# Kernel optimization log

Measured on AMD Instinct MI355X. Metric: run time of the kernel, lower is better.

## Reference

```python
import jax, jax.numpy as jnp
import numpy as np

STRIDES = {"feat1": 4, "feat2": 8, "feat3": 16}
ROI_SIZES = {"feat1": 28, "feat2": 14, "feat3": 7}
SAMPLING_RATIO = 2


def roi_align(feat, rois, out_size, spatial_scale, ratio):
    """torchvision roi_align with aligned=True, fixed sampling_ratio.
    feat: (B,C,H,W); rois: (N,5) [batch_idx,x1,y1,x2,y2]. Returns (N,C,P,P)."""
    B, C, H, W = feat.shape
    bidx = rois[:, 0].astype(jnp.int32)
    # aligned=True: half-pixel offset
    x1 = rois[:, 1] * spatial_scale - 0.5
    y1 = rois[:, 2] * spatial_scale - 0.5
    x2 = rois[:, 3] * spatial_scale - 0.5
    y2 = rois[:, 4] * spatial_scale - 0.5
    bin_h = (y2 - y1) / out_size
    bin_w = (x2 - x1) / out_size
    # per-bin sampling grid offsets: (P, r)
    grid = jnp.arange(out_size, dtype=feat.dtype)[:, None] + \
        (jnp.arange(ratio, dtype=feat.dtype)[None, :] + 0.5) / ratio
    ys = y1[:, None, None] + grid[None] * bin_h[:, None, None]  # (N,P,ry)
    xs = x1[:, None, None] + grid[None] * bin_w[:, None, None]  # (N,P,rx)
    yy = ys[:, :, :, None, None]  # (N,P,ry,1,1)
    xx = xs[:, None, None, :, :]  # (N,1,1,P,rx)
    valid = (yy > -1.0) & (yy < H) & (xx > -1.0) & (xx < W)
    yc = jnp.clip(yy, 0.0, H - 1.0)
    xc = jnp.clip(xx, 0.0, W - 1.0)
    y0 = jnp.floor(yc).astype(jnp.int32)
    x0 = jnp.floor(xc).astype(jnp.int32)
    y1i = jnp.minimum(y0 + 1, H - 1)
    x1i = jnp.minimum(x0 + 1, W - 1)
    ly = yc - y0
    lx = xc - x0
    hy = 1.0 - ly
    hx = 1.0 - lx
    b = bidx[:, None, None, None, None]  # (N,1,1,1,1)

    def gather(yi, xi):
        # advanced indexing -> (N,P,ry,P,rx,C)
        return feat[b, :, yi, xi]

    v = ((hy * hx)[..., None] * gather(y0, x0)
         + (hy * lx)[..., None] * gather(y0, x1i)
         + (ly * hx)[..., None] * gather(y1i, x0)
         + (ly * lx)[..., None] * gather(y1i, x1i))
    v = jnp.where(valid[..., None], v, 0.0)
    out = v.mean(axis=(2, 4))  # average over sampling grid -> (N,P,P,C)
    return jnp.transpose(out, (0, 3, 1, 2))  # (N,C,P,P)


def setup_inputs() -> dict:
    key = jax.random.key(0)
    ks = jax.random.split(key, 6)
    B, C, N, IMG = 2, 256, 128, 1024
    feat1 = jax.random.normal(ks[0], (B, C, 256, 256), jnp.float32)
    feat2 = jax.random.normal(ks[1], (B, C, 128, 128), jnp.float32)
    feat3 = jax.random.normal(ks[2], (B, C, 64, 64), jnp.float32)
    bidx = jax.random.randint(ks[3], (N,), 0, B).astype(jnp.float32)
    xy1 = jax.random.uniform(ks[4], (N, 2), jnp.float32, 0.0, IMG - 64.0)
    wh = jax.random.uniform(ks[5], (N, 2), jnp.float32, 16.0, 320.0)
    xy2 = jnp.minimum(xy1 + wh, IMG - 1.0)
    rois = jnp.concatenate(
        [bidx[:, None], xy1[:, :1], xy1[:, 1:], xy2[:, :1], xy2[:, 1:]], axis=1)
    return {"feat1": feat1, "feat2": feat2, "feat3": feat3, "rois": rois}


def reference(feat1, feat2, feat3, rois):
    feats = {"feat1": feat1, "feat2": feat2, "feat3": feat3}
    return tuple(
        roi_align(feats[k], rois, ROI_SIZES[k], 1.0 / STRIDES[k], SAMPLING_RATIO)
        for k in ("feat1", "feat2", "feat3"))
```

## Files before the change

kernel.cpp:

```cpp
#include <hip/hip_runtime.h>

#define C_CH 256

__global__ __launch_bounds__(256) void nchw_to_nhwc(
    const float* __restrict__ in, float* __restrict__ out, int HW)
{
    __shared__ float lds[64 * 64];
    int ct = blockIdx.y & 3;
    int b  = blockIdx.y >> 2;
    int hw0 = blockIdx.x << 6;
    int c0  = ct << 6;
    const float* ip = in  + (size_t)b * C_CH * HW;
    float*       op = out + (size_t)b * HW * C_CH;

    int t   = threadIdx.x;
    int q   = t & 15;
    int r0  = t >> 4;

#pragma unroll
    for (int k = 0; k < 4; ++k) {
        int c_local = r0 + (k << 4);
        const float4 v = *reinterpret_cast<const float4*>(
            ip + (size_t)(c0 + c_local) * HW + hw0 + (q << 2));
#pragma unroll
        for (int i = 0; i < 4; ++i) {
            int hw_local = (q << 2) + i;
            lds[(hw_local << 6) + ((c_local + hw_local) & 63)] = ((const float*)&v)[i];
        }
    }
    __syncthreads();
#pragma unroll
    for (int k = 0; k < 4; ++k) {
        int hw_local = r0 + (k << 4);
        float4 v;
#pragma unroll
        for (int j = 0; j < 4; ++j) {
            int c_local = (q << 2) + j;
            ((float*)&v)[j] = lds[(hw_local << 6) + ((c_local + hw_local) & 63)];
        }
        *reinterpret_cast<float4*>(
            op + (size_t)(hw0 + hw_local) * C_CH + c0 + (q << 2)) = v;
    }
}

template<int P, int POS>
__global__ __launch_bounds__(256) void roi_gather_nhwc(
    const float* __restrict__ nhwc, const float* __restrict__ rois,
    float* __restrict__ out, int H, int W, float scale)
{
    constexpr int PITCH = 260;
    __shared__ float lds[POS * PITCH];

    const int n   = blockIdx.x;
    const int ph0 = blockIdx.y * (POS / P);
    const int lane = threadIdx.x & 63;
    const int wid  = threadIdx.x >> 6;
    const int c4   = lane << 2;

    const float* r = rois + n * 5;
    const int b = (int)r[0];
    const float x1 = fmaf(r[1], scale, -0.5f);
    const float y1 = fmaf(r[2], scale, -0.5f);
    const float x2 = fmaf(r[3], scale, -0.5f);
    const float y2 = fmaf(r[4], scale, -0.5f);
    const float bin_h = (y2 - y1) * (1.0f / P);
    const float bin_w = (x2 - x1) * (1.0f / P);

    const float Hm1 = (float)(H - 1), Wm1 = (float)(W - 1);
    const float Hf = (float)H, Wf = (float)W;
    const float* fb = nhwc + (size_t)b * H * W * C_CH;

    for (int pos = wid; pos < POS; pos += 4) {
        int ph = ph0 + pos / P;
        int pw = pos % P;

        float w[16];
        int   offc[16];
#pragma unroll
        for (int iy = 0; iy < 2; ++iy) {
            float gy = (float)ph + (iy ? 0.75f : 0.25f);
            float yy = fmaf(gy, bin_h, y1);
            bool vy = (yy > -1.0f) && (yy < Hf);
            float yc = fminf(fmaxf(yy, 0.0f), Hm1);
            float y0f = floorf(yc);
            int   y0  = (int)y0f;
            float ly  = yc - y0f, hy = 1.0f - ly;
            int   y1i = min(y0 + 1, H - 1);
            int ro0 = y0 * W, ro1 = y1i * W;
#pragma unroll
            for (int ix = 0; ix < 2; ++ix) {
                float gx = (float)pw + (ix ? 0.75f : 0.25f);
                float xx = fmaf(gx, bin_w, x1);
                bool v = vy && (xx > -1.0f) && (xx < Wf);
                float xc = fminf(fmaxf(xx, 0.0f), Wm1);
                float x0f = floorf(xc);
                int   x0  = (int)x0f;
                float lx  = xc - x0f, hx = 1.0f - lx;
                int   x1i = min(x0 + 1, W - 1);
                float q = v ? 0.25f : 0.0f;
                int s = ((iy << 1) + ix) << 2;
                w[s + 0] = hy * hx * q;  offc[s + 0] = ((ro0 + x0 ) << 8) + c4;
                w[s + 1] = hy * lx * q;  offc[s + 1] = ((ro0 + x1i) << 8) + c4;
                w[s + 2] = ly * hx * q;  offc[s + 2] = ((ro1 + x0 ) << 8) + c4;
                w[s + 3] = ly * lx * q;  offc[s + 3] = ((ro1 + x1i) << 8) + c4;
            }
        }

        float4 acc = {0.f, 0.f, 0.f, 0.f};
#pragma unroll
        for (int m = 0; m < 16; ++m) {
            const float4 v = *reinterpret_cast<const float4*>(fb + (size_t)(unsigned)offc[m]);
            acc.x = fmaf(w[m], v.x, acc.x);
            acc.y = fmaf(w[m], v.y, acc.y);
            acc.z = fmaf(w[m], v.z, acc.z);
            acc.w = fmaf(w[m], v.w, acc.w);
        }
        *reinterpret_cast<float4*>(&lds[pos * PITCH + c4]) = acc;
    }
    __syncthreads();

    const size_t obase = (size_t)n * C_CH * P * P + (size_t)ph0 * P;
    for (int i = threadIdx.x; i < C_CH * POS; i += 256) {
        int c = i / POS;
        int pos = i - c * POS;
        out[obase + (size_t)c * (P * P) + pos] = lds[pos * PITCH + c];
    }
}

template<int P, int CPT>
__global__ __launch_bounds__(256) void roi_align_direct(
    const float* __restrict__ feat, const float* __restrict__ rois,
    float* __restrict__ out, int N, int H, int W, float scale)
{
    constexpr int CG = C_CH / CPT;
    int tid = blockIdx.x * blockDim.x + threadIdx.x;
    int total = N * CG * P * P;
    if (tid >= total) return;

    int pw = tid % P;
    int t  = tid / P;
    int ph = t % P;
    t /= P;
    int cg = t % CG;
    int n  = t / CG;

    const float* r = rois + n * 5;
    int b = (int)r[0];
    float x1 = fmaf(r[1], scale, -0.5f);
    float y1 = fmaf(r[2], scale, -0.5f);
    float x2 = fmaf(r[3], scale, -0.5f);
    float y2 = fmaf(r[4], scale, -0.5f);
    float bin_h = (y2 - y1) * (1.0f / P);
    float bin_w = (x2 - x1) * (1.0f / P);

    float acc[CPT];
#pragma unroll
    for (int j = 0; j < CPT; ++j) acc[j] = 0.0f;

    const int HW = H * W;
    const float* fp = feat + ((size_t)b * C_CH + (size_t)cg * CPT) * HW;
    const float Hm1 = (float)(H - 1), Wm1 = (float)(W - 1);
    const float Hf = (float)H, Wf = (float)W;

#pragma unroll
    for (int iy = 0; iy < 2; ++iy) {
        float gy = (float)ph + (iy ? 0.75f : 0.25f);
        float yy = fmaf(gy, bin_h, y1);
        bool vy = (yy > -1.0f) && (yy < Hf);
        float yc = fminf(fmaxf(yy, 0.0f), Hm1);
        float y0f = floorf(yc);
        int   y0  = (int)y0f;
        float ly  = yc - y0f, hy = 1.0f - ly;
        int   y1i = min(y0 + 1, H - 1);
        int ro0 = y0 * W, ro1 = y1i * W;
#pragma unroll
        for (int ix = 0; ix < 2; ++ix) {
            float gx = (float)pw + (ix ? 0.75f : 0.25f);
            float xx = fmaf(gx, bin_w, x1);
            bool v = vy && (xx > -1.0f) && (xx < Wf);
            float xc = fminf(fmaxf(xx, 0.0f), Wm1);
            float x0f = floorf(xc);
            int   x0  = (int)x0f;
            float lx  = xc - x0f, hx = 1.0f - lx;
            int   x1i = min(x0 + 1, W - 1);
            float q = v ? 0.25f : 0.0f;
            float w00 = hy * hx * q, w01 = hy * lx * q;
            float w10 = ly * hx * q, w11 = ly * lx * q;
            int o00 = ro0 + x0, o01 = ro0 + x1i;
            int o10 = ro1 + x0, o11 = ro1 + x1i;
#pragma unroll
            for (int j = 0; j < CPT; ++j) {
                const float* pj = fp + j * HW;
                acc[j] = fmaf(w00, pj[o00], acc[j]);
                acc[j] = fmaf(w01, pj[o01], acc[j]);
                acc[j] = fmaf(w10, pj[o10], acc[j]);
                acc[j] = fmaf(w11, pj[o11], acc[j]);
            }
        }
    }

    float* op = out + (((size_t)n * C_CH + (size_t)cg * CPT) * P + ph) * P + pw;
#pragma unroll
    for (int j = 0; j < CPT; ++j) op[(size_t)j * P * P] = acc[j];
}

extern "C" void kernel_launch(void* const* d_in, const int* in_sizes, int n_in,
                              void* d_out, int out_size, void* d_ws, size_t ws_size,
                              hipStream_t stream) {
    const float* feat1 = (const float*)d_in[0];
    const float* feat2 = (const float*)d_in[1];
    const float* feat3 = (const float*)d_in[2];
    const float* rois  = (const float*)d_in[3];
    const int N = in_sizes[3] / 5;

    float* out1 = (float*)d_out;
    float* out2 = out1 + (size_t)N * C_CH * 28 * 28;
    float* out3 = out2 + (size_t)N * C_CH * 14 * 14;

    const size_t e1 = (size_t)2 * C_CH * 256 * 256;
    const size_t e2 = (size_t)2 * C_CH * 128 * 128;
    const size_t e3 = (size_t)2 * C_CH * 64 * 64;

    size_t off = 0;
    float* t1 = nullptr; float* t2 = nullptr; float* t3 = nullptr;
    if (off + e1 * 4 <= ws_size) { t1 = (float*)d_ws + off / 4 * 0 + off / sizeof(float); off += e1 * 4; }
    if (off + e2 * 4 <= ws_size) { t2 = (float*)((char*)d_ws + off); off += e2 * 4; }
    if (off + e3 * 4 <= ws_size) { t3 = (float*)((char*)d_ws + off); off += e3 * 4; }
    if (t1) t1 = (float*)d_ws;

    if (t1) nchw_to_nhwc<<<dim3(65536 / 64, 8), 256, 0, stream>>>(feat1, t1, 65536);
    if (t2) nchw_to_nhwc<<<dim3(16384 / 64, 8), 256, 0, stream>>>(feat2, t2, 16384);
    if (t3) nchw_to_nhwc<<<dim3( 4096 / 64, 8), 256, 0, stream>>>(feat3, t3,  4096);

    if (t1) {
        roi_gather_nhwc<28, 28><<<dim3(N, 28), 256, 0, stream>>>(t1, rois, out1, 256, 256, 0.25f);
    } else {
        int total = N * (C_CH / 4) * 28 * 28;
        roi_align_direct<28, 4><<<(total + 255) / 256, 256, 0, stream>>>(feat1, rois, out1, N, 256, 256, 0.25f);
    }
    if (t2) {
        roi_gather_nhwc<14, 28><<<dim3(N, 7), 256, 0, stream>>>(t2, rois, out2, 128, 128, 0.125f);
    } else {
        int total = N * (C_CH / 4) * 14 * 14;
        roi_align_direct<14, 4><<<(total + 255) / 256, 256, 0, stream>>>(feat2, rois, out2, N, 128, 128, 0.125f);
    }
    if (t3) {
        roi_gather_nhwc<7, 49><<<dim3(N, 1), 256, 0, stream>>>(t3, rois, out3, 64, 64, 0.0625f);
    } else {
        int total = N * (C_CH / 4) * 7 * 7;
        roi_align_direct<7, 4><<<(total + 255) / 256, 256, 0, stream>>>(feat3, rois, out3, N, 64, 64, 0.0625f);
    }
}
```

Baseline: 435.8 us.

## Batch gather loads, XCD-aware block remap, swizzled LDS with vectorized output stores

The gather kernel now issues all 16 float4 loads before the FMAs, with a sched_barrier between them to raise memory-level parallelism. Block IDs are remapped so blocks sharing an ROI land on the same XCD for L2 reuse. The LDS transpose buffer uses an XOR swizzle so the output writes can be float4-vectorized for P=28 and P=14. It also adds launch_bounds occupancy hints and refactors the weight and offset computation into a helper. The trade-off is higher register pressure from holding 16 float4 loads at once.

```diff
diff --git a/kernel.cpp b/kernel.cpp
--- a/kernel.cpp
+++ b/kernel.cpp
@@ -43,125 +43,12 @@
     }
 }
 
-template<int P, int POS>
-__global__ __launch_bounds__(256) void roi_gather_nhwc(
-    const float* __restrict__ nhwc, const float* __restrict__ rois,
-    float* __restrict__ out, int H, int W, float scale)
-{
-    constexpr int PITCH = 260;
-    __shared__ float lds[POS * PITCH];
-
-    const int n   = blockIdx.x;
-    const int ph0 = blockIdx.y * (POS / P);
-    const int lane = threadIdx.x & 63;
-    const int wid  = threadIdx.x >> 6;
-    const int c4   = lane << 2;
-
-    const float* r = rois + n * 5;
-    const int b = (int)r[0];
-    const float x1 = fmaf(r[1], scale, -0.5f);
-    const float y1 = fmaf(r[2], scale, -0.5f);
-    const float x2 = fmaf(r[3], scale, -0.5f);
-    const float y2 = fmaf(r[4], scale, -0.5f);
-    const float bin_h = (y2 - y1) * (1.0f / P);
-    const float bin_w = (x2 - x1) * (1.0f / P);
-
+__device__ __forceinline__ void woff16(
+    int ph, int pw, float y1, float x1, float bin_h, float bin_w,
+    int H, int W, int c4, float* __restrict__ w, int* __restrict__ off)
+{
     const float Hm1 = (float)(H - 1), Wm1 = (float)(W - 1);
     const float Hf = (float)H, Wf = (float)W;
-    const float* fb = nhwc + (size_t)b * H * W * C_CH;
-
-    for (int pos = wid; pos < POS; pos += 4) {
-        int ph = ph0 + pos / P;
-        int pw = pos % P;
-
-        float w[16];
-        int   offc[16];
-#pragma unroll
-        for (int iy = 0; iy < 2; ++iy) {
-            float gy = (float)ph + (iy ? 0.75f : 0.25f);
-            float yy = fmaf(gy, bin_h, y1);
-            bool vy = (yy > -1.0f) && (yy < Hf);
-            float yc = fminf(fmaxf(yy, 0.0f), Hm1);
-            float y0f = floorf(yc);
-            int   y0  = (int)y0f;
-            float ly  = yc - y0f, hy = 1.0f - ly;
-            int   y1i = min(y0 + 1, H - 1);
-            int ro0 = y0 * W, ro1 = y1i * W;
-#pragma unroll
-            for (int ix = 0; ix < 2; ++ix) {
-                float gx = (float)pw + (ix ? 0.75f : 0.25f);
-                float xx = fmaf(gx, bin_w, x1);
-                bool v = vy && (xx > -1.0f) && (xx < Wf);
-                float xc = fminf(fmaxf(xx, 0.0f), Wm1);
-                float x0f = floorf(xc);
-                int   x0  = (int)x0f;
-                float lx  = xc - x0f, hx = 1.0f - lx;
-                int   x1i = min(x0 + 1, W - 1);
-                float q = v ? 0.25f : 0.0f;
-                int s = ((iy << 1) + ix) << 2;
-                w[s + 0] = hy * hx * q;  offc[s + 0] = ((ro0 + x0 ) << 8) + c4;
-                w[s + 1] = hy * lx * q;  offc[s + 1] = ((ro0 + x1i) << 8) + c4;
-                w[s + 2] = ly * hx * q;  offc[s + 2] = ((ro1 + x0 ) << 8) + c4;
-                w[s + 3] = ly * lx * q;  offc[s + 3] = ((ro1 + x1i) << 8) + c4;
-            }
-        }
-
-        float4 acc = {0.f, 0.f, 0.f, 0.f};
-#pragma unroll
-        for (int m = 0; m < 16; ++m) {
-            const float4 v = *reinterpret_cast<const float4*>(fb + (size_t)(unsigned)offc[m]);
-            acc.x = fmaf(w[m], v.x, acc.x);
-            acc.y = fmaf(w[m], v.y, acc.y);
-            acc.z = fmaf(w[m], v.z, acc.z);
-            acc.w = fmaf(w[m], v.w, acc.w);
-        }
-        *reinterpret_cast<float4*>(&lds[pos * PITCH + c4]) = acc;
-    }
-    __syncthreads();
-
-    const size_t obase = (size_t)n * C_CH * P * P + (size_t)ph0 * P;
-    for (int i = threadIdx.x; i < C_CH * POS; i += 256) {
-        int c = i / POS;
-        int pos = i - c * POS;
-        out[obase + (size_t)c * (P * P) + pos] = lds[pos * PITCH + c];
-    }
-}
-
-template<int P, int CPT>
-__global__ __launch_bounds__(256) void roi_align_direct(
-    const float* __restrict__ feat, const float* __restrict__ rois,
-    float* __restrict__ out, int N, int H, int W, float scale)
-{
-    constexpr int CG = C_CH / CPT;
-    int tid = blockIdx.x * blockDim.x + threadIdx.x;
-    int total = N * CG * P * P;
-    if (tid >= total) return;
-
-    int pw = tid % P;
-    int t  = tid / P;
-    int ph = t % P;
-    t /= P;
-    int cg = t % CG;
-    int n  = t / CG;
-
-    const float* r = rois + n * 5;
-    int b = (int)r[0];
-    float x1 = fmaf(r[1], scale, -0.5f);
-    float y1 = fmaf(r[2], scale, -0.5f);
-    float x2 = fmaf(r[3], scale, -0.5f);
-    float y2 = fmaf(r[4], scale, -0.5f);
-    float bin_h = (y2 - y1) * (1.0f / P);
-    float bin_w = (x2 - x1) * (1.0f / P);
-
-    float acc[CPT];
-#pragma unroll
-    for (int j = 0; j < CPT; ++j) acc[j] = 0.0f;
-
-    const int HW = H * W;
-    const float* fp = feat + ((size_t)b * C_CH + (size_t)cg * CPT) * HW;
-    const float Hm1 = (float)(H - 1), Wm1 = (float)(W - 1);
-    const float Hf = (float)H, Wf = (float)W;
-
 #pragma unroll
     for (int iy = 0; iy < 2; ++iy) {
         float gy = (float)ph + (iy ? 0.75f : 0.25f);
@@ -184,19 +71,137 @@
             float lx  = xc - x0f, hx = 1.0f - lx;
             int   x1i = min(x0 + 1, W - 1);
             float q = v ? 0.25f : 0.0f;
-            float w00 = hy * hx * q, w01 = hy * lx * q;
-            float w10 = ly * hx * q, w11 = ly * lx * q;
-            int o00 = ro0 + x0, o01 = ro0 + x1i;
-            int o10 = ro1 + x0, o11 = ro1 + x1i;
-#pragma unroll
-            for (int j = 0; j < CPT; ++j) {
-                const float* pj = fp + j * HW;
-                acc[j] = fmaf(w00, pj[o00], acc[j]);
-                acc[j] = fmaf(w01, pj[o01], acc[j]);
-                acc[j] = fmaf(w10, pj[o10], acc[j]);
-                acc[j] = fmaf(w11, pj[o11], acc[j]);
+            int s = ((iy << 1) + ix) << 2;
+            w[s + 0] = hy * hx * q;  off[s + 0] = ((ro0 + x0 ) << 8) + c4;
+            w[s + 1] = hy * lx * q;  off[s + 1] = ((ro0 + x1i) << 8) + c4;
+            w[s + 2] = ly * hx * q;  off[s + 2] = ((ro1 + x0 ) << 8) + c4;
+            w[s + 3] = ly * lx * q;  off[s + 3] = ((ro1 + x1i) << 8) + c4;
+        }
+    }
+}
+
+template<int P, int POS>
+__global__ __launch_bounds__(256, 3) void roi_gather_nhwc(
+    const float* __restrict__ nhwc, const float* __restrict__ rois,
+    float* __restrict__ out, int H, int W, float scale, int N)
+{
+    constexpr int PITCH = 260;
+    constexpr int NB = (P * P) / POS;
+    __shared__ float lds[POS * PITCH];
+
+    const int G = N * NB;
+    int bid = blockIdx.x;
+    int virt = (G % 8 == 0) ? ((bid & 7) * (G >> 3) + (bid >> 3)) : bid;
+    int n  = virt / NB;
+    int rb = virt - n * NB;
+    int ph0 = rb * (POS / P);
+
+    const int lane = threadIdx.x & 63;
+    const int wid  = threadIdx.x >> 6;
+    const int c4   = lane << 2;
+
+    const float* r = rois + n * 5;
+    const int b = (int)r[0];
+    const float x1 = fmaf(r[1], scale, -0.5f);
+    const float y1 = fmaf(r[2], scale, -0.5f);
+    const float x2 = fmaf(r[3], scale, -0.5f);
+    const float y2 = fmaf(r[4], scale, -0.5f);
+    const float bin_h = (y2 - y1) * (1.0f / P);
+    const float bin_w = (x2 - x1) * (1.0f / P);
+    const float* fb = nhwc + (size_t)b * H * W * C_CH;
+
+    for (int pos = wid; pos < POS; pos += 4) {
+        int ph = ph0 + pos / P;
+        int pw = pos % P;
+
+        float w[16];
+        int   off[16];
+        woff16(ph, pw, y1, x1, bin_h, bin_w, H, W, c4, w, off);
+
+        float4 v[16];
+#pragma unroll
+        for (int m = 0; m < 16; ++m)
+            v[m] = *reinterpret_cast<const float4*>(fb + (size_t)(unsigned)off[m]);
+        __builtin_amdgcn_sched_barrier(0);
+
+        float4 acc = {0.f, 0.f, 0.f, 0.f};
+#pragma unroll
+        for (int m = 0; m < 16; ++m) {
+            acc.x = fmaf(w[m], v[m].x, acc.x);
+            acc.y = fmaf(w[m], v[m].y, acc.y);
+            acc.z = fmaf(w[m], v[m].z, acc.z);
+            acc.w = fmaf(w[m], v[m].w, acc.w);
+        }
+        int slot = ((c4 >> 2) ^ (pos & 7)) << 2;
+        *reinterpret_cast<float4*>(&lds[pos * PITCH + slot]) = acc;
+    }
+    __syncthreads();
+
+    const size_t obase = (size_t)n * C_CH * (P * P) + (size_t)ph0 * P;
+    if constexpr (P != 7) {
+        constexpr int K4 = POS / 4;
+        for (int i = threadIdx.x; i < C_CH * K4; i += 256) {
+            int c  = i / K4;
+            int k4 = i - c * K4;
+            float4 o;
+#pragma unroll
+            for (int j = 0; j < 4; ++j) {
+                int pos = (k4 << 2) + j;
+                ((float*)&o)[j] = lds[pos * PITCH + ((((c >> 2) ^ (pos & 7)) << 2) | (c & 3))];
             }
-        }
+            *reinterpret_cast<float4*>(out + obase + (size_t)c * (P * P) + (k4 << 2)) = o;
+        }
+    } else {
+        for (int i = threadIdx.x; i < C_CH * POS; i += 256) {
+            int c   = i / POS;
+            int pos = i - c * POS;
+            out[obase + (size_t)c * (P * P) + pos] =
+                lds[pos * PITCH + ((((c >> 2) ^ (pos & 7)) << 2) | (c & 3))];
+        }
+    }
+}
+
+template<int P, int CPT>
+__global__ __launch_bounds__(256) void roi_align_direct(
+    const float* __restrict__ feat, const float* __restrict__ rois,
+    float* __restrict__ out, int N, int H, int W, float scale)
+{
+    constexpr int CG = C_CH / CPT;
+    int tid = blockIdx.x * blockDim.x + threadIdx.x;
+    int total = N * CG * P * P;
+    if (tid >= total) return;
+
+    int pw = tid % P;
+    int t  = tid / P;
+    int ph = t % P;
+    t /= P;
+    int cg = t % CG;
+    int n  = t / CG;
+
+    const float* r = rois + n * 5;
+    int b = (int)r[0];
+    float x1 = fmaf(r[1], scale, -0.5f);
+    float y1 = fmaf(r[2], scale, -0.5f);
+    float x2 = fmaf(r[3], scale, -0.5f);
+    float y2 = fmaf(r[4], scale, -0.5f);
+    float bin_h = (y2 - y1) * (1.0f / P);
+    float bin_w = (x2 - x1) * (1.0f / P);
+
+    float acc[CPT];
+#pragma unroll
+    for (int j = 0; j < CPT; ++j) acc[j] = 0.0f;
+
+    const int HW = H * W;
+    const float* fp = feat + ((size_t)b * C_CH + (size_t)cg * CPT) * HW;
+
+    float w[16]; int off[16];
+    woff16(ph, pw, y1, x1, bin_h, bin_w, H, W, 0, w, off);
+#pragma unroll
+    for (int m = 0; m < 16; ++m) {
+        int sp = off[m] >> 8;
+#pragma unroll
+        for (int j = 0; j < CPT; ++j)
+            acc[j] = fmaf(w[m], fp[(size_t)j * HW + sp], acc[j]);
     }
 
     float* op = out + (((size_t)n * C_CH + (size_t)cg * CPT) * P + ph) * P + pw;
@@ -223,29 +228,28 @@
 
     size_t off = 0;
     float* t1 = nullptr; float* t2 = nullptr; float* t3 = nullptr;
-    if (off + e1 * 4 <= ws_size) { t1 = (float*)d_ws + off / 4 * 0 + off / sizeof(float); off += e1 * 4; }
+    if (off + e1 * 4 <= ws_size) { t1 = (float*)((char*)d_ws + off); off += e1 * 4; }
     if (off + e2 * 4 <= ws_size) { t2 = (float*)((char*)d_ws + off); off += e2 * 4; }
     if (off + e3 * 4 <= ws_size) { t3 = (float*)((char*)d_ws + off); off += e3 * 4; }
-    if (t1) t1 = (float*)d_ws;
 
     if (t1) nchw_to_nhwc<<<dim3(65536 / 64, 8), 256, 0, stream>>>(feat1, t1, 65536);
     if (t2) nchw_to_nhwc<<<dim3(16384 / 64, 8), 256, 0, stream>>>(feat2, t2, 16384);
     if (t3) nchw_to_nhwc<<<dim3( 4096 / 64, 8), 256, 0, stream>>>(feat3, t3,  4096);
 
     if (t1) {
-        roi_gather_nhwc<28, 28><<<dim3(N, 28), 256, 0, stream>>>(t1, rois, out1, 256, 256, 0.25f);
+        roi_gather_nhwc<28, 28><<<N * 28, 256, 0, stream>>>(t1, rois, out1, 256, 256, 0.25f, N);
     } else {
         int total = N * (C_CH / 4) * 28 * 28;
         roi_align_direct<28, 4><<<(total + 255) / 256, 256, 0, stream>>>(feat1, rois, out1, N, 256, 256, 0.25f);
     }
     if (t2) {
-        roi_gather_nhwc<14, 28><<<dim3(N, 7), 256, 0, stream>>>(t2, rois, out2, 128, 128, 0.125f);
+        roi_gather_nhwc<14, 28><<<N * 7, 256, 0, stream>>>(t2, rois, out2, 128, 128, 0.125f, N);
     } else {
         int total = N * (C_CH / 4) * 14 * 14;
         roi_align_direct<14, 4><<<(total + 255) / 256, 256, 0, stream>>>(feat2, rois, out2, N, 128, 128, 0.125f);
     }
     if (t3) {
-        roi_gather_nhwc<7, 49><<<dim3(N, 1), 256, 0, stream>>>(t3, rois, out3, 64, 64, 0.0625f);
+        roi_gather_nhwc<7, 49><<<N * 1, 256, 0, stream>>>(t3, rois, out3, 64, 64, 0.0625f, N);
     } else {
         int total = N * (C_CH / 4) * 7 * 7;
         roi_align_direct<7, 4><<<(total + 255) / 256, 256, 0, stream>>>(feat3, rois, out3, N, 64, 64, 0.0625f);
```

New measurement: 423.3 us. -2.9%, faster.
